# Performance work log

Hardware: AMD Instinct MI355X
Metric: run time of the kernel (lower is better)

Reference implementation:

```python
import jax, jax.numpy as jnp
import numpy as np

G_OFF = 1e-6
G_ON = 1e-4
K_V = 0.5
BATCH, SIZE_IN, SIZE_OUT = 512, 2048, 2048


def setup_inputs() -> dict:
    key = jax.random.key(0)
    k1, k2 = jax.random.split(key)
    stdv = 1.0 / np.sqrt(SIZE_IN)
    x = jax.random.normal(k1, (BATCH, SIZE_IN), dtype=jnp.float32)
    weights = jax.random.normal(k2, (SIZE_OUT, SIZE_IN), dtype=jnp.float32) * stdv
    bias = jnp.zeros((SIZE_OUT,), dtype=jnp.float32)
    return {"x": x, "weights": weights, "bias": bias}


def reference(x, weights, bias):
    # inputs with bias column of ones: (B, in+1)
    inputs = jnp.concatenate([x, jnp.ones((x.shape[0], 1), dtype=x.dtype)], axis=1)
    # weights_and_bias: (in+1, out)
    wb = jnp.concatenate([weights.T, bias[None, :]], axis=0)

    V = K_V * inputs                               # (B, in+1)
    max_wb = jnp.max(jnp.abs(wb))
    k_G = (G_ON - G_OFF) / max_wb
    k_I = K_V * k_G
    G_eff = k_G * wb
    G_pos = G_OFF + jnp.maximum(G_eff, 0.0)        # (in+1, out)
    G_neg = G_OFF - jnp.minimum(G_eff, 0.0)        # (in+1, out)

    # The torch code builds an interleaved G of shape (in+1, 2*out), computes
    # I_ind = V[:,:,None] * G[None,:,:], sums over the input axis, then takes
    # even - odd columns. That is exactly V @ G_pos - V @ G_neg.
    I_total = V @ G_pos - V @ G_neg                # (B, out)
    return I_total / k_I
```

## Files before the change

kernel.cpp:

```cpp
#include <hip/hip_runtime.h>
#include <hip/hip_bf16.h>


typedef float  float4_t __attribute__((ext_vector_type(4)));
typedef short  short8_t __attribute__((ext_vector_type(8)));
typedef float  floatx4  __attribute__((ext_vector_type(4)));

constexpr int M = 512, N = 2048, K = 2048;
constexpr int BM = 64, BN = 64, BK = 64;
constexpr int LDK = BK + 8;

__global__ __launch_bounds__(256)
void memristor_gemm(const float* __restrict__ x, const float* __restrict__ w,
                    const float* __restrict__ bias, float* __restrict__ out)
{
    __shared__ __hip_bfloat16 As[BM][LDK];
    __shared__ __hip_bfloat16 Bs[BN][LDK];

    const int tid  = threadIdx.x;
    const int bn   = blockIdx.x;
    const int bm   = blockIdx.y;
    const int lane = tid & 63;
    const int wave = tid >> 6;
    const int wm   = (wave >> 1) * 32;
    const int wn   = (wave & 1) * 32;
    const int l16  = lane & 15;
    const int quad = lane >> 4;

    floatx4 acc[2][2];
    #pragma unroll
    for (int i = 0; i < 2; ++i)
        #pragma unroll
        for (int j = 0; j < 2; ++j)
            acc[i][j] = (floatx4){0.f, 0.f, 0.f, 0.f};

    const int sr = tid >> 4;
    const int sc = (tid & 15) << 2;

    const float* xrow = x + (size_t)(bm * BM + sr) * K + sc;
    const float* wrow = w + (size_t)(bn * BN + sr) * K + sc;

    for (int k0 = 0; k0 < K; k0 += BK) {
        float4_t va[4], vb[4];
        #pragma unroll
        for (int p = 0; p < 4; ++p) {
            va[p] = *(const float4_t*)(xrow + (size_t)(p * 16) * K + k0);
            vb[p] = *(const float4_t*)(wrow + (size_t)(p * 16) * K + k0);
        }
        #pragma unroll
        for (int p = 0; p < 4; ++p) {
            const int r = p * 16 + sr;
            union { __hip_bfloat16 h[4]; unsigned long long u; } ua, ub;
            ua.h[0] = __float2bfloat16(va[p].x);
            ua.h[1] = __float2bfloat16(va[p].y);
            ua.h[2] = __float2bfloat16(va[p].z);
            ua.h[3] = __float2bfloat16(va[p].w);
            ub.h[0] = __float2bfloat16(vb[p].x);
            ub.h[1] = __float2bfloat16(vb[p].y);
            ub.h[2] = __float2bfloat16(vb[p].z);
            ub.h[3] = __float2bfloat16(vb[p].w);
            *(unsigned long long*)&As[r][sc] = ua.u;
            *(unsigned long long*)&Bs[r][sc] = ub.u;
        }
        __syncthreads();

        #pragma unroll
        for (int kk = 0; kk < BK; kk += 32) {
            short8_t af[2], bf[2];
            #pragma unroll
            for (int t = 0; t < 2; ++t) {
                af[t] = *(const short8_t*)(&As[wm + t * 16 + l16][kk + quad * 8]);
                bf[t] = *(const short8_t*)(&Bs[wn + t * 16 + l16][kk + quad * 8]);
            }
            #pragma unroll
            for (int i = 0; i < 2; ++i)
                #pragma unroll
                for (int j = 0; j < 2; ++j)
                    acc[i][j] = __builtin_amdgcn_mfma_f32_16x16x32_bf16(
                        af[i], bf[j], acc[i][j], 0, 0, 0);
        }
        __syncthreads();
    }

    #pragma unroll
    for (int j = 0; j < 2; ++j) {
        const int col = bn * BN + wn + j * 16 + l16;
        const float bv = bias[col];
        #pragma unroll
        for (int i = 0; i < 2; ++i) {
            const int row0 = bm * BM + wm + i * 16 + quad * 4;
            #pragma unroll
            for (int r = 0; r < 4; ++r)
                out[(size_t)(row0 + r) * N + col] = acc[i][j][r] + bv;
        }
    }
}

extern "C" void kernel_launch(void* const* d_in, const int* in_sizes, int n_in,
                              void* d_out, int out_size, void* d_ws, size_t ws_size,
                              hipStream_t stream) {
    const float* x    = (const float*)d_in[0];
    const float* w    = (const float*)d_in[1];
    const float* bias = (const float*)d_in[2];
    float* out = (float*)d_out;

    dim3 grid(N / BN, M / BM);
    memristor_gemm<<<grid, 256, 0, stream>>>(x, w, bias, out);
}
```

Measured before the change: 96.78 us.

## Double-buffer LDS tiles with register prefetch and split-K across wave pairs

Doubles BK to 128 and double-buffers the shared-memory tiles, prefetching the next global tile into registers while the current tile is computed, so only one barrier is needed per iteration. The block grows to 512 threads, and two groups of four waves each handle half of the K slice. Their partial accumulators are reduced through shared memory before the bias is added and the result stored. This aims to hide global load latency and raise waves per block, at the cost of more LDS, an extra reduction step and higher register pressure.

```diff
diff --git a/kernel.cpp b/kernel.cpp
--- a/kernel.cpp
+++ b/kernel.cpp
@@ -7,25 +7,33 @@
 typedef float  floatx4  __attribute__((ext_vector_type(4)));
 
 constexpr int M = 512, N = 2048, K = 2048;
-constexpr int BM = 64, BN = 64, BK = 64;
+constexpr int BM = 64, BN = 64, BK = 128;
 constexpr int LDK = BK + 8;
+constexpr int NT  = K / BK;
 
-__global__ __launch_bounds__(256)
+__global__ __launch_bounds__(512)
 void memristor_gemm(const float* __restrict__ x, const float* __restrict__ w,
                     const float* __restrict__ bias, float* __restrict__ out)
 {
-    __shared__ __hip_bfloat16 As[BM][LDK];
-    __shared__ __hip_bfloat16 Bs[BN][LDK];
+    __shared__ __hip_bfloat16 As[2][BM][LDK];
+    __shared__ __hip_bfloat16 Bs[2][BN][LDK];
 
     const int tid  = threadIdx.x;
-    const int bn   = blockIdx.x;
-    const int bm   = blockIdx.y;
+    const int bn   = blockIdx.x, bm = blockIdx.y;
     const int lane = tid & 63;
     const int wave = tid >> 6;
-    const int wm   = (wave >> 1) * 32;
-    const int wn   = (wave & 1) * 32;
+    const int wsp  = wave & 3;
+    const int kp   = wave >> 2;
+    const int wm   = (wsp >> 1) * 32;
+    const int wn   = (wsp & 1) * 32;
     const int l16  = lane & 15;
     const int quad = lane >> 4;
+
+    const int srow = tid >> 5;
+    const int sc4  = tid & 31;
+
+    const float* xp = x + (size_t)(bm * BM + srow) * K + sc4 * 4;
+    const float* wp = w + (size_t)(bn * BN + srow) * K + sc4 * 4;
 
     floatx4 acc[2][2];
     #pragma unroll
@@ -34,44 +42,43 @@
         for (int j = 0; j < 2; ++j)
             acc[i][j] = (floatx4){0.f, 0.f, 0.f, 0.f};
 
-    const int sr = tid >> 4;
-    const int sc = (tid & 15) << 2;
+    float4_t va[4], vb[4];
 
-    const float* xrow = x + (size_t)(bm * BM + sr) * K + sc;
-    const float* wrow = w + (size_t)(bn * BN + sr) * K + sc;
+    auto load_tile = [&](int t) {
+        #pragma unroll
+        for (int r = 0; r < 4; ++r) {
+            va[r] = *(const float4_t*)(xp + (size_t)r * 16 * K + t * BK);
+            vb[r] = *(const float4_t*)(wp + (size_t)r * 16 * K + t * BK);
+        }
+    };
 
-    for (int k0 = 0; k0 < K; k0 += BK) {
-        float4_t va[4], vb[4];
+    auto stage = [&](int buf) {
         #pragma unroll
-        for (int p = 0; p < 4; ++p) {
-            va[p] = *(const float4_t*)(xrow + (size_t)(p * 16) * K + k0);
-            vb[p] = *(const float4_t*)(wrow + (size_t)(p * 16) * K + k0);
+        for (int r = 0; r < 4; ++r) {
+            const int row = r * 16 + srow;
+            union { __hip_bfloat16 h[4]; unsigned long long u; } ua, ub;
+            ua.h[0] = __float2bfloat16(va[r].x);
+            ua.h[1] = __float2bfloat16(va[r].y);
+            ua.h[2] = __float2bfloat16(va[r].z);
+            ua.h[3] = __float2bfloat16(va[r].w);
+            ub.h[0] = __float2bfloat16(vb[r].x);
+            ub.h[1] = __float2bfloat16(vb[r].y);
+            ub.h[2] = __float2bfloat16(vb[r].z);
+            ub.h[3] = __float2bfloat16(vb[r].w);
+            *(unsigned long long*)&As[buf][row][sc4 * 4] = ua.u;
+            *(unsigned long long*)&Bs[buf][row][sc4 * 4] = ub.u;
         }
+    };
+
+    auto compute = [&](int buf) {
         #pragma unroll
-        for (int p = 0; p < 4; ++p) {
-            const int r = p * 16 + sr;
-            union { __hip_bfloat16 h[4]; unsigned long long u; } ua, ub;
-            ua.h[0] = __float2bfloat16(va[p].x);
-            ua.h[1] = __float2bfloat16(va[p].y);
-            ua.h[2] = __float2bfloat16(va[p].z);
-            ua.h[3] = __float2bfloat16(va[p].w);
-            ub.h[0] = __float2bfloat16(vb[p].x);
-            ub.h[1] = __float2bfloat16(vb[p].y);
-            ub.h[2] = __float2bfloat16(vb[p].z);
-            ub.h[3] = __float2bfloat16(vb[p].w);
-            *(unsigned long long*)&As[r][sc] = ua.u;
-            *(unsigned long long*)&Bs[r][sc] = ub.u;
-        }
-        __syncthreads();
-
-        #pragma unroll
-        for (int kk = 0; kk < BK; kk += 32) {
+        for (int s = 0; s < 2; ++s) {
+            const int kb = kp * 64 + s * 32 + quad * 8;
             short8_t af[2], bf[2];
-            #pragma unroll
-            for (int t = 0; t < 2; ++t) {
-                af[t] = *(const short8_t*)(&As[wm + t * 16 + l16][kk + quad * 8]);
-                bf[t] = *(const short8_t*)(&Bs[wn + t * 16 + l16][kk + quad * 8]);
-            }
+            af[0] = *(const short8_t*)&As[buf][wm + l16][kb];
+            af[1] = *(const short8_t*)&As[buf][wm + 16 + l16][kb];
+            bf[0] = *(const short8_t*)&Bs[buf][wn + l16][kb];
+            bf[1] = *(const short8_t*)&Bs[buf][wn + 16 + l16][kb];
             #pragma unroll
             for (int i = 0; i < 2; ++i)
                 #pragma unroll
@@ -79,19 +86,48 @@
                     acc[i][j] = __builtin_amdgcn_mfma_f32_16x16x32_bf16(
                         af[i], bf[j], acc[i][j], 0, 0, 0);
         }
+    };
+
+    load_tile(0);
+    stage(0);
+    load_tile(1);
+    __syncthreads();
+
+    for (int t = 0; t < NT; ++t) {
+        const int cur = t & 1;
+        compute(cur);
+        if (t + 1 < NT) {
+            stage(cur ^ 1);
+            if (t + 2 < NT) load_tile(t + 2);
+        }
         __syncthreads();
     }
 
-    #pragma unroll
-    for (int j = 0; j < 2; ++j) {
-        const int col = bn * BN + wn + j * 16 + l16;
-        const float bv = bias[col];
+    float* scrb = (float*)&As[0][0][0];
+    if (kp == 1) {
         #pragma unroll
-        for (int i = 0; i < 2; ++i) {
-            const int row0 = bm * BM + wm + i * 16 + quad * 4;
+        for (int i = 0; i < 2; ++i)
             #pragma unroll
-            for (int r = 0; r < 4; ++r)
-                out[(size_t)(row0 + r) * N + col] = acc[i][j][r] + bv;
+            for (int j = 0; j < 2; ++j) {
+                float* p = scrb + ((wsp * 32 + j * 16 + l16) * 36 + i * 16 + quad * 4);
+                *(floatx4*)p = acc[i][j];
+            }
+    }
+    __syncthreads();
+    if (kp == 0) {
+        #pragma unroll
+        for (int j = 0; j < 2; ++j) {
+            const int col = bn * BN + wn + j * 16 + l16;
+            const float bv = bias[col];
+            #pragma unroll
+            for (int i = 0; i < 2; ++i) {
+                const floatx4 part = *(const floatx4*)(
+                    scrb + ((wsp * 32 + j * 16 + l16) * 36 + i * 16 + quad * 4));
+                const int row0 = bm * BM + wm + i * 16 + quad * 4;
+                #pragma unroll
+                for (int r = 0; r < 4; ++r)
+                    out[(size_t)(row0 + r) * N + col] = acc[i][j][r] + part[r] + bv;
+            }
         }
     }
 }
@@ -105,5 +141,5 @@
     float* out = (float*)d_out;
 
     dim3 grid(N / BN, M / BM);
-    memristor_gemm<<<grid, 256, 0, stream>>>(x, w, bias, out);
+    memristor_gemm<<<grid, 512, 0, stream>>>(x, w, bias, out);
 }
```

Result: faster. 81.89 us (-15.4%).
